# Kernel tuning notes

Measured on AMD Instinct MI355X. Metric: run time of the kernel, lower is better.

## Reference

```python
import jax, jax.numpy as jnp
import numpy as np
from jax import lax

L, B, T_IMG, T_TXT = 12, 2, 256, 64
E, H, G = 1024, 16, 2730
V = 16416  # image_vocab_count + 1
C = E // H
EPS = 1e-6  # flax LayerNorm default


def _ln(x, scale, bias):
    mu = jnp.mean(x, -1, keepdims=True)
    var = jnp.var(x, -1, keepdims=True)
    y = (x - mu) * lax.rsqrt(var + EPS)
    if scale is not None:
        y = y * scale
    if bias is not None:
        y = y + bias
    return y


def _attend(k, v, q, mask, o_w):
    # k,v: [B,K,H,C]  q: [B,Q,H,C]  mask: [B,K]
    bias = jnp.where(mask, 0.0, -jnp.inf)[:, None, None, :]
    w = jnp.einsum('bqhc,bkhc->bhqk', q, k) + bias
    w = jax.nn.softmax(w, axis=-1)
    out = jnp.einsum('bhqk,bkhc->bqhc', w, v)
    return out.reshape(out.shape[0], out.shape[1], E) @ o_w


def setup_inputs():
    key = jax.random.key(0)
    ks = jax.random.split(key, 16)
    s = 0.02
    n = lambda k, shape: jax.random.normal(k, shape, jnp.float32) * s
    return dict(
        encoder_state=n(ks[0], (B, T_TXT, E)),
        keys_state=jnp.zeros((L, B, T_IMG, H, C), jnp.float32),
        values_state=jnp.zeros((L, B, T_IMG, H, C), jnp.float32),
        attention_mask=jnp.ones((B, T_TXT), jnp.bool_),
        prev_token=5000,
        token_index=100,
        embed_tok=n(ks[1], (V, E)),
        embed_pos=n(ks[2], (T_IMG, E)),
        ln_emb_s=jnp.ones((E,), jnp.float32),
        ln_emb_b=jnp.zeros((E,), jnp.float32),
        final_ln_b=jnp.zeros((E,), jnp.float32),
        lm_head_w=n(ks[3], (E, V)),
        pre_sa_ln_b=jnp.zeros((L, E), jnp.float32),
        sa_q_w=n(ks[4], (L, E, E)), sa_k_w=n(ks[5], (L, E, E)),
        sa_v_w=n(ks[6], (L, E, E)), sa_o_w=n(ks[7], (L, E, E)),
        sa_ln_s=jnp.ones((L, E), jnp.float32), sa_ln_b=jnp.zeros((L, E), jnp.float32),
        pre_ca_ln_b=jnp.zeros((L, E), jnp.float32),
        ca_q_w=n(ks[8], (L, E, E)), ca_k_w=n(ks[9], (L, E, E)),
        ca_v_w=n(ks[10], (L, E, E)), ca_o_w=n(ks[11], (L, E, E)),
        ca_ln_s=jnp.ones((L, E), jnp.float32), ca_ln_b=jnp.zeros((L, E), jnp.float32),
        glu_ln0_b=jnp.zeros((L, E), jnp.float32),
        glu_fc0_w=n(ks[12], (L, E, G)), glu_fc1_w=n(ks[13], (L, E, G)),
        glu_ln1_b=jnp.zeros((L, G), jnp.float32),
        glu_fc2_w=n(ks[14], (L, G, E)),
    )


def _decode_step(encoder_state, keys_state, values_state, attention_mask,
                 prev_token, token_index, embed_tok, embed_pos,
                 ln_emb_s, ln_emb_b, final_ln_b, lm_head_w, layer_params):
    ones = jnp.ones((B, 1), jnp.int32)
    ds = embed_tok[prev_token * ones] + embed_pos[token_index * ones]  # [B,1,E]
    ds = _ln(ds, ln_emb_s, ln_emb_b)
    self_mask = jnp.broadcast_to(jnp.arange(T_IMG) < token_index + 1, (B, T_IMG))
    scale = C ** 0.5

    def step(ds, xs):
        ks_l, vs_l, p = xs  # per-layer KV cache [B,T_IMG,H,C] and params
        (pre_sa_b, qw, kw, vw, ow, sa_s, sa_b,
         pre_ca_b, cqw, ckw, cvw, cow, ca_s, ca_b,
         g0b, f0, f1, g1b, f2) = p
        # --- self attention with KV-cache append ---
        residual = ds
        x = _ln(ds, None, pre_sa_b)
        ks_l = lax.dynamic_update_slice(ks_l, (x @ kw).reshape(B, 1, H, C), (0, token_index, 0, 0))
        vs_l = lax.dynamic_update_slice(vs_l, (x @ vw).reshape(B, 1, H, C), (0, token_index, 0, 0))
        q = (x @ qw).reshape(B, 1, H, C) / scale
        x = _attend(ks_l, vs_l, q, self_mask, ow)
        ds = residual + _ln(x, sa_s, sa_b)
        # --- cross attention over encoder state ---
        residual = ds
        x = _ln(ds, None, pre_ca_b)
        ek = (encoder_state @ ckw).reshape(B, T_TXT, H, C)
        ev = (encoder_state @ cvw).reshape(B, T_TXT, H, C)
        q = (x @ cqw).reshape(B, 1, H, C) / scale
        x = _attend(ek, ev, q, attention_mask, cow)
        ds = residual + _ln(x, ca_s, ca_b)
        # --- GLU FFN ---
        residual = ds
        z = _ln(ds, None, g0b)
        w = jax.nn.gelu(z @ f0, approximate=False)
        z = _ln(w * (z @ f1), None, g1b)
        ds = residual + z @ f2
        return ds, (ks_l, vs_l)

    ds, (keys_state, values_state) = lax.scan(step, ds, (keys_state, values_state, layer_params))
    ds = _ln(ds, None, final_ln_b)
    logits = ds @ lm_head_w  # [B,1,V]
    return logits, keys_state, values_state


def reference(encoder_state, keys_state, values_state, attention_mask, prev_token,
              token_index, embed_tok, embed_pos, ln_emb_s, ln_emb_b, final_ln_b,
              lm_head_w, pre_sa_ln_b, sa_q_w, sa_k_w, sa_v_w, sa_o_w, sa_ln_s,
              sa_ln_b, pre_ca_ln_b, ca_q_w, ca_k_w, ca_v_w, ca_o_w, ca_ln_s,
              ca_ln_b, glu_ln0_b, glu_fc0_w, glu_fc1_w, glu_ln1_b, glu_fc2_w):
    layer_params = (pre_sa_ln_b, sa_q_w, sa_k_w, sa_v_w, sa_o_w, sa_ln_s, sa_ln_b,
                    pre_ca_ln_b, ca_q_w, ca_k_w, ca_v_w, ca_o_w, ca_ln_s, ca_ln_b,
                    glu_ln0_b, glu_fc0_w, glu_fc1_w, glu_ln1_b, glu_fc2_w)
    return _decode_step(encoder_state, keys_state, values_state, attention_mask,
                        prev_token, token_index, embed_tok, embed_pos,
                        ln_emb_s, ln_emb_b, final_ln_b, lm_head_w, layer_params)
```

## Files before the change

kernel.cpp:

```cpp
#include <hip/hip_runtime.h>
#include <math.h>

#define LAYERS 12
#define EE 1024
#define GG 2730
#define VV 16416
#define EPS 1e-6f

#define OFF_DS 0
#define NSLOT 37
#define OFF_ACC (OFF_DS + NSLOT*2048)
#define ACC_STRIDE 28672
#define AQ 0
#define AK 2048
#define AV 4096
#define AY 6144
#define ASC 10240
#define AY2 14336
#define AA 16384
#define AB2 21844
#define ACC_TOTAL (LAYERS*ACC_STRIDE)

#define KVL 524288
#define KVB 262144

struct MegaP {
  const float* enc; const float* keys_in; const float* values_in;
  const int* maski; const int* pt; const int* ti;
  const float* tok; const float* pos; const float* ln_s; const float* ln_b;
  const float* final_b; const float* lm_w;
  const float* pre_sa_b; const float* saq; const float* sak; const float* sav;
  const float* sao; const float* sas; const float* sab;
  const float* pre_ca_b; const float* caq; const float* ckw; const float* cvw;
  const float* cao; const float* cas; const float* cab;
  const float* g0b; const float* f0; const float* f1; const float* g1b; const float* f2;
  float* logits; float* keys_out; float* values_out; float* ws;
};

__device__ __forceinline__ void red4(float* sm, float& a, float& b, float& c, float& d){
  #pragma unroll
  for(int o=32;o;o>>=1){ a+=__shfl_down(a,o); b+=__shfl_down(b,o); c+=__shfl_down(c,o); d+=__shfl_down(d,o); }
  int w=threadIdx.x>>6, l=threadIdx.x&63;
  __syncthreads();
  if(l==0){ sm[w]=a; sm[4+w]=b; sm[8+w]=c; sm[12+w]=d; }
  __syncthreads();
  a=sm[0]+sm[1]+sm[2]+sm[3]; b=sm[4]+sm[5]+sm[6]+sm[7];
  c=sm[8]+sm[9]+sm[10]+sm[11]; d=sm[12]+sm[13]+sm[14]+sm[15];
}

__device__ __forceinline__ void ln_stats_g(const float* v, int K, float* sm,
    float& mu0, float& rs0, float& mu1, float& rs1){
  float s0=0,q0=0,s1=0,q1=0;
  for(int i=threadIdx.x;i<K;i+=256){ float a=v[i], b=v[K+i]; s0+=a;q0+=a*a;s1+=b;q1+=b*b; }
  red4(sm,s0,q0,s1,q1);
  mu0=s0/K; mu1=s1/K;
  rs0=rsqrtf(fmaxf(q0/K-mu0*mu0,0.f)+EPS);
  rs1=rsqrtf(fmaxf(q1/K-mu1*mu1,0.f)+EPS);
}

__device__ __forceinline__ void ln_stats_l(float (*Ds)[1024], float* sm,
    float& mu0, float& rs0, float& mu1, float& rs1){
  float s0=0,q0=0,s1=0,q1=0;
  for(int i=threadIdx.x;i<EE;i+=256){ float a=Ds[0][i], b=Ds[1][i]; s0+=a;q0+=a*a;s1+=b;q1+=b*b; }
  red4(sm,s0,q0,s1,q1);
  mu0=s0/EE; mu1=s1/EE;
  rs0=rsqrtf(fmaxf(q0/EE-mu0*mu0,0.f)+EPS);
  rs1=rsqrtf(fmaxf(q1/EE-mu1*mu1,0.f)+EPS);
}

__device__ __forceinline__ void build_ds3(const float* dsi, const float* accL,
    const float* sasl, const float* sabl, const float* casl, const float* cabl,
    float (*Ds)[1024], float* sm){
  float mu0,rs0,mu1,rs1;
  ln_stats_g(accL+AY, EE, sm, mu0,rs0,mu1,rs1);
  for(int i=threadIdx.x;i<EE;i+=256){ float sc=sasl[i], bi=sabl[i];
    Ds[0][i]=dsi[i]    + (accL[AY+i]-mu0)*rs0*sc + bi;
    Ds[1][i]=dsi[EE+i] + (accL[AY+EE+i]-mu1)*rs1*sc + bi; }
  ln_stats_g(accL+AY2, EE, sm, mu0,rs0,mu1,rs1);
  for(int i=threadIdx.x;i<EE;i+=256){ float sc=casl[i], bi=cabl[i];
    Ds[0][i] += (accL[AY2+i]-mu0)*rs0*sc + bi;
    Ds[1][i] += (accL[AY2+EE+i]-mu1)*rs1*sc + bi; }
}

__global__ __launch_bounds__(256)
void k_prelude(MegaP p){
  __shared__ float ev[EE];
  __shared__ float sm[16];
  const int t=threadIdx.x, b=blockIdx.x;
  if (b==0){
    int ptv = p.pt[0], tiv = p.ti[0];
    float s0=0,q0=0,d1=0,d2=0;
    for(int i=t;i<EE;i+=256){ float v=p.tok[(size_t)ptv*EE+i]+p.pos[(size_t)tiv*EE+i]; ev[i]=v; s0+=v; q0+=v*v; }
    red4(sm,s0,q0,d1,d2);
    float mu=s0/EE, rs=rsqrtf(fmaxf(q0/EE-mu*mu,0.f)+EPS);
    float* ds0 = p.ws + OFF_DS;
    __syncthreads();
    for(int i=t;i<EE;i+=256){ float y=(ev[i]-mu)*rs*p.ln_s[i]+p.ln_b[i]; ds0[i]=y; ds0[EE+i]=y; }
  } else {
    int idx = (b-1)*256 + t;
    for (int i=idx; i<2*VV; i+=9984) p.logits[i]=0.f;
    float* a0 = p.ws + OFF_ACC;
    for (int i=idx; i<ACC_STRIDE; i+=9984) a0[i]=0.f;
    float* d3 = p.ws + OFF_DS + 3*2048;
    for (int i=idx; i<2048; i+=9984) d3[i]=0.f;
  }
}

__global__ __launch_bounds__(256)
void k_qkv(MegaP p, int l){
  __shared__ float Xs[2][1024];
  __shared__ float sm[16];
  const int t=threadIdx.x, bx=blockIdx.x, by=blockIdx.y;
  if (bx >= 12){
    int cb = (bx-12)*64 + by;
    #pragma unroll
    for(int j=0;j<4;j++){
      int idx4 = cb*1024 + j*256 + t;
      int kv = idx4 >> 17;
      int r4 = idx4 & 131071;
      size_t off = (size_t)l*KVL + (size_t)r4*4;
      float4 v = *(const float4*)((kv? p.values_in : p.keys_in) + off);
      *(float4*)((kv? p.values_out : p.keys_out) + off) = v;
    }
    if (l < 11){
      int zi = cb*256 + t;
      float* an = p.ws + OFF_ACC + (size_t)(l+1)*ACC_STRIDE;
      if (zi < ACC_STRIDE) an[zi]=0.f;
      float* dn = p.ws + OFF_DS + (size_t)(3*l+6)*2048;
      if (zi < 2048) dn[zi]=0.f;
    }
    return;
  }
  const float* dsi = p.ws + OFF_DS + (size_t)(3*l)*2048;
  float* accL = p.ws + OFF_ACC + (size_t)l*ACC_STRIDE;
  const size_t lE2=(size_t)l*EE*EE, lE=(size_t)l*EE;
  int c = bx*256 + t;
  int sel = c>>10, cc = c&1023;
  const float* W = (sel==0? p.saq : sel==1? p.sak : p.sav) + lE2;
  float* O = accL + (sel==0? AQ : sel==1? AK : AV);
  int k0 = by*16;
  const float* wp = W + (size_t)k0*EE + cc;
  float wr[16];
  #pragma unroll
  for(int k=0;k<16;k++) wr[k] = wp[(size_t)k*EE];
  float mu0,rs0,mu1,rs1;
  ln_stats_g(dsi, EE, sm, mu0,rs0,mu1,rs1);
  for(int i=t;i<EE;i+=256){ float bi=p.pre_sa_b[lE+i];
    Xs[0][i]=(dsi[i]-mu0)*rs0+bi; Xs[1][i]=(dsi[EE+i]-mu1)*rs1+bi; }
  __syncthreads();
  float a0=0,a1=0;
  #pragma unroll
  for(int k=0;k<16;k++){ a0+=Xs[0][k0+k]*wr[k]; a1+=Xs[1][k0+k]*wr[k]; }
  atomicAdd(&O[cc],a0); atomicAdd(&O[EE+cc],a1);
}

__global__ __launch_bounds__(256)
void k_selfo(MegaP p, int l){
  __shared__ float Ds[2][1024];
  __shared__ float att[2][256];
  __shared__ float sm[16];
  const int t=threadIdx.x, bkid=blockIdx.x, tiv=p.ti[0];
  float* accL = p.ws + OFF_ACC + (size_t)l*ACC_STRIDE;
  const size_t lE2=(size_t)l*EE*EE;
  int cg=bkid&3, h=(bkid>>2)&15, sub=(bkid>>6)&3, hoff=h*64;
  if (t < 128){ int bb2=t>>6, c2=t&63; Ds[bb2][c2] = accL[AQ + bb2*EE + hoff + c2]*0.125f; }
  __syncthreads();
  for(int bb2=0;bb2<2;bb2++)
    for(int tt=t; tt<=tiv; tt+=256){
      const float* kr = (tt<tiv) ? (p.keys_in + (size_t)l*KVL + (size_t)bb2*KVB + (size_t)tt*EE + hoff)
                                 : (accL + AK + bb2*EE + hoff);
      float d=0;
      #pragma unroll
      for(int c2=0;c2<64;c2++) d += Ds[bb2][c2]*kr[c2];
      att[bb2][tt] = d;
    }
  __syncthreads();
  int wv=t>>6, l2=t&63;
  if (wv<2){
    float m=-3.4e38f;
    for(int tt=l2; tt<=tiv; tt+=64) m=fmaxf(m, att[wv][tt]);
    #pragma unroll
    for(int o=32;o;o>>=1) m=fmaxf(m,__shfl_xor(m,o));
    float s=0;
    for(int tt=l2; tt<=tiv; tt+=64){ float e=__expf(att[wv][tt]-m); att[wv][tt]=e; s+=e; }
    #pragma unroll
    for(int o=32;o;o>>=1) s+=__shfl_xor(s,o);
    if(l2==0) sm[8+wv]=1.f/s;
  }
  __syncthreads();
  {
    int bb2=t>>7, j=(t>>3)&15, part=t&7, colh=sub*16+j;
    float v=0;
    for(int tt=part; tt<=tiv; tt+=8){
      float vv = (tt<tiv)? p.values_in[(size_t)l*KVL + (size_t)bb2*KVB + (size_t)tt*EE + hoff + colh]
                         : accL[AV + bb2*EE + hoff + colh];
      v += att[bb2][tt]*vv;
    }
    v += __shfl_down(v,4,8); v += __shfl_down(v,2,8); v += __shfl_down(v,1,8);
    if(part==0) Ds[bb2][512+j] = v*sm[8+bb2];
  }
  __syncthreads();
  {
    int c = cg*256+t, kb = hoff + sub*16;
    const float* wp = p.sao + lE2 + (size_t)kb*EE + c;
    float a0=0,a1=0;
    #pragma unroll
    for(int j2=0;j2<16;j2++){ float w=wp[(size_t)j2*EE]; a0+=Ds[0][512+j2]*w; a1+=Ds[1][512+j2]*w; }
    atomicAdd(&accL[AY+c],a0); atomicAdd(&accL[AY+EE+c],a1);
  }
  if (cg==0 && sub==0){
    int bb2=t>>7, kv=(t>>6)&1, c2=t&63;
    float val = accL[(kv?AV:AK) + bb2*EE + hoff + c2];
    float* dst = (kv? p.values_out : p.keys_out)
               + (size_t)l*KVL + (size_t)bb2*KVB + (size_t)tiv*EE + hoff + c2;
    *dst = val;
  }
}

__global__ __launch_bounds__(256)
void k_qscore(MegaP p, int l){
  __shared__ float Xs[1024];
  __shared__ float P[16][64];
  __shared__ float qs[64];
  __shared__ float us[256];
  __shared__ float sm[16];
  const int t=threadIdx.x, bh=blockIdx.x, ec=blockIdx.y;
  const int b=bh>>4, h=bh&15, hoff=h*64;
  float* accL = p.ws + OFF_ACC + (size_t)l*ACC_STRIDE;
  const float* dsi = p.ws + OFF_DS + (size_t)(3*l)*2048;
  const size_t lE2=(size_t)l*EE*EE, lE=(size_t)l*EE;
  const int w=t>>6, ln=t&63;

  float s0=0,q0=0;
  for(int i=t;i<EE;i+=256){ float v=accL[AY+b*EE+i]; s0+=v; q0+=v*v; }
  #pragma unroll
  for(int o=32;o;o>>=1){ s0+=__shfl_down(s0,o); q0+=__shfl_down(q0,o); }
  if(ln==0){ sm[w]=s0; sm[4+w]=q0; }
  __syncthreads();
  float mu=(sm[0]+sm[1]+sm[2]+sm[3])/EE;
  float qq=(sm[4]+sm[5]+sm[6]+sm[7])/EE;
  float rs=rsqrtf(fmaxf(qq-mu*mu,0.f)+EPS);
  float s1=0,q1=0;
  for(int i=t;i<EE;i+=256){
    float d = dsi[b*EE+i] + (accL[AY+b*EE+i]-mu)*rs*p.sas[lE+i] + p.sab[lE+i];
    Xs[i]=d; s1+=d; q1+=d*d;
  }
  #pragma unroll
  for(int o=32;o;o>>=1){ s1+=__shfl_down(s1,o); q1+=__shfl_down(q1,o); }
  if(ln==0){ sm[8+w]=s1; sm[12+w]=q1; }
  __syncthreads();
  float mu2=(sm[8]+sm[9]+sm[10]+sm[11])/EE;
  float q2=(sm[12]+sm[13]+sm[14]+sm[15])/EE;
  float rs2=rsqrtf(fmaxf(q2-mu2*mu2,0.f)+EPS);
  for(int i=t;i<EE;i+=256) Xs[i] = (Xs[i]-mu2)*rs2 + p.pre_ca_b[lE+i];
  __syncthreads();

  {
    int c4=t&15, kr=t>>4;
    const float4* cq = (const float4*)(p.caq + lE2 + (size_t)kr*EE + hoff) + c4;
    float ax=0,ay=0,az=0,aw=0;
    #pragma unroll 8
    for(int i=0;i<64;i++){
      float4 wv = cq[(size_t)i*16*256];
      float x = Xs[kr+16*i];
      ax+=x*wv.x; ay+=x*wv.y; az+=x*wv.z; aw+=x*wv.w;
    }
    P[kr][c4*4+0]=ax; P[kr][c4*4+1]=ay; P[kr][c4*4+2]=az; P[kr][c4*4+3]=aw;
  }
  __syncthreads();
  if (t<64){
    float qv=0;
    #pragma unroll
    for(int kr=0;kr<16;kr++) qv += P[kr][t];
    qs[t] = qv*0.125f;
  }
  __syncthreads();

  {
    const float4* ckp = (const float4*)(p.ckw + lE2 + (size_t)(ec*256+t)*EE + hoff);
    float u=0;
    #pragma unroll
    for(int j=0;j<16;j++){
      float4 wv=ckp[j];
      u += wv.x*qs[4*j] + wv.y*qs[4*j+1] + wv.z*qs[4*j+2] + wv.w*qs[4*j+3];
    }
    us[t]=u;
  }
  __syncthreads();

  int t2=t&63, q4=t>>6;
  const float4* ep = (const float4*)(p.enc + (size_t)(b*64+t2)*EE + ec*256 + q4*64);
  float pa=0;
  #pragma unroll
  for(int j=0;j<16;j++){
    float4 e4=ep[j];
    pa += e4.x*us[q4*64+4*j] + e4.y*us[q4*64+4*j+1] + e4.z*us[q4*64+4*j+2] + e4.w*us[q4*64+4*j+3];
  }
  atomicAdd(&accL[ASC + (b*16+h)*64 + t2], pa);
}

__global__ __launch_bounds__(256)
void k_ovy2(MegaP p, int l){
  __shared__ float att[64];
  __shared__ float ctxp[2][128];
  __shared__ float ctxs[128];
  __shared__ float P[256];
  __shared__ float outh[64];
  const int t=threadIdx.x, bh=blockIdx.x, es=blockIdx.y;
  const int b=bh>>4, h=bh&15, hoff=h*64, e0=es*128;
  float* accL = p.ws + OFF_ACC + (size_t)l*ACC_STRIDE;
  const size_t lE2=(size_t)l*EE*EE;
  const int c=t&63, part=t>>6;
  const float* vp = p.cvw + lE2 + (size_t)(e0+part*32)*EE + hoff + c;
  float wr[32];
  #pragma unroll
  for(int j=0;j<32;j++) wr[j] = vp[(size_t)j*EE];
  if (t<64){
    float sc = accL[ASC + (b*16+h)*64 + t];
    int mi=b*64+t;
    bool valid = (p.maski[mi]!=0) || (((const unsigned char*)p.maski)[mi]!=0);
    sc = valid? sc : -3.4e38f;
    float m=sc;
    #pragma unroll
    for(int o=32;o;o>>=1) m=fmaxf(m,__shfl_xor(m,o));
    float e_ = valid? __expf(sc-m) : 0.f;
    float s=e_;
    #pragma unroll
    for(int o=32;o;o>>=1) s+=__shfl_xor(s,o);
    att[t]=e_/s;
  }
  __syncthreads();
  {
    int e2=t>>1, half=t&1;
    const float* ep = p.enc + (size_t)(b*64+half*32)*EE + e0+e2;
    float ca=0;
    #pragma unroll 8
    for(int tt=0;tt<32;tt++) ca += att[half*32+tt]*ep[(size_t)tt*EE];
    ctxp[half][e2]=ca;
  }
  __syncthreads();
  if (t<128) ctxs[t] = ctxp[0][t]+ctxp[1][t];
  __syncthreads();
  {
    float po=0;
    #pragma unroll
    for(int j=0;j<32;j++) po += ctxs[part*32+j]*wr[j];
    P[t]=po;
  }
  __syncthreads();
  if (t<64) outh[t] = P[t]+P[64+t]+P[128+t]+P[192+t];
  __syncthreads();
  {
    const float* cop = p.cao + lE2 + (size_t)hoff*EE;
    for(int n=t;n<EE;n+=256){
      float y=0;
      #pragma unroll 8
      for(int c2=0;c2<64;c2++) y += outh[c2]*cop[(size_t)c2*EE + n];
      atomicAdd(&accL[AY2 + b*EE + n], y);
    }
  }
}

__global__ __launch_bounds__(256)
void k_glu01(MegaP p, int l){
  __shared__ float Xs[2][1024];
  __shared__ float Ds[2][1024];
  __shared__ float sm[16];
  const int t=threadIdx.x;
  const float* dsi = p.ws + OFF_DS + (size_t)(3*l)*2048;
  float* accL = p.ws + OFF_ACC + (size_t)l*ACC_STRIDE;
  const size_t lEG=(size_t)l*EE*GG, lE=(size_t)l*EE;
  int c2 = blockIdx.x*256 + t;
  int k0 = blockIdx.y*16;
  int sel=0, col=0;
  const float* W = nullptr;
  float2 wr[16];
  if (c2 < 2730){
    sel = (c2>=1365); int cc2 = sel? c2-1365 : c2; col = cc2*2;
    W = (sel? p.f1 : p.f0) + lEG;
    const float2* wp = (const float2*)(W + (size_t)k0*GG + col);
    #pragma unroll
    for(int k=0;k<16;k++) wr[k] = wp[(size_t)k*1365];
  }
  build_ds3(dsi, accL, p.sas+lE, p.sab+lE, p.cas+lE, p.cab+lE, Ds, sm);
  float mu0,rs0,mu1,rs1;
  ln_stats_l(Ds, sm, mu0,rs0,mu1,rs1);
  for(int i=t;i<EE;i+=256){ float bi=p.g0b[lE+i];
    Xs[0][i]=(Ds[0][i]-mu0)*rs0+bi; Xs[1][i]=(Ds[1][i]-mu1)*rs1+bi; }
  __syncthreads();
  if (c2 < 2730){
    float* O = accL + (sel? AB2 : AA);
    float a0=0,a1=0,b0=0,b1=0;
    #pragma unroll
    for(int k=0;k<16;k++){
      float x0=Xs[0][k0+k], x1=Xs[1][k0+k];
      a0+=x0*wr[k].x; a1+=x0*wr[k].y; b0+=x1*wr[k].x; b1+=x1*wr[k].y;
    }
    atomicAdd(&O[col+0],a0); atomicAdd(&O[col+1],a1);
    atomicAdd(&O[GG+col+0],b0); atomicAdd(&O[GG+col+1],b1);
  }
}

__global__ __launch_bounds__(256)
void k_glu2(MegaP p, int l){
  __shared__ float Xs[2][2736];
  __shared__ float Ds[2][1024];
  __shared__ float sm[16];
  const int t=threadIdx.x;
  const float* dsi = p.ws + OFF_DS + (size_t)(3*l)*2048;
  float* ds4 = p.ws + OFF_DS + (size_t)(3*l+3)*2048;
  float* accL = p.ws + OFF_ACC + (size_t)l*ACC_STRIDE;
  const size_t lGE=(size_t)l*GG*EE, lE=(size_t)l*EE, lG=(size_t)l*GG;
  const int ks = blockIdx.y;
  int c = blockIdx.x*256 + t;
  int k0 = ks*32, k1 = k0+32; if (k1>GG) k1=GG;
  const float* wp = p.f2 + lGE + (size_t)k0*EE + c;
  float wr[32];
  #pragma unroll
  for(int k=0;k<32;k++) wr[k] = (k0+k<GG) ? wp[(size_t)k*EE] : 0.f;
  if (ks==0) build_ds3(dsi, accL, p.sas+lE, p.sab+lE, p.cas+lE, p.cab+lE, Ds, sm);
  float s0=0,q0=0,s1=0,q1=0;
  for(int i=t;i<GG;i+=256){
    float a0v=accL[AA+i], a1v=accL[AA+GG+i];
    float b0v=accL[AB2+i], b1v=accL[AB2+GG+i];
    float g0v=0.5f*a0v*(1.f+erff(a0v*0.70710678118654752f));
    float g1v=0.5f*a1v*(1.f+erff(a1v*0.70710678118654752f));
    float t0=g0v*b0v, t1=g1v*b1v;
    Xs[0][i]=t0; Xs[1][i]=t1;
    s0+=t0;q0+=t0*t0;s1+=t1;q1+=t1*t1;
  }
  red4(sm,s0,q0,s1,q1);
  float mu0=s0/GG, mu1=s1/GG;
  float rs0=rsqrtf(fmaxf(q0/GG-mu0*mu0,0.f)+EPS), rs1=rsqrtf(fmaxf(q1/GG-mu1*mu1,0.f)+EPS);
  for(int i=t;i<GG;i+=256){ float bi=p.g1b[lG+i];
    Xs[0][i]=(Xs[0][i]-mu0)*rs0+bi; Xs[1][i]=(Xs[1][i]-mu1)*rs1+bi; }
  __syncthreads();
  float a0=0,b0=0;
  if (ks==0){ a0=Ds[0][c]; b0=Ds[1][c]; }
  #pragma unroll
  for(int k=0;k<32;k++){
    if (k0+k<GG){ a0+=Xs[0][k0+k]*wr[k]; b0+=Xs[1][k0+k]*wr[k]; }
  }
  atomicAdd(&ds4[c],a0); atomicAdd(&ds4[EE+c],b0);
}

__global__ __launch_bounds__(256)
void k_lm(MegaP p){
  __shared__ float Xs[2][1024];
  __shared__ float sm[16];
  const int t=threadIdx.x;
  const float* dsf = p.ws + OFF_DS + (size_t)36*2048;
  float mu0,rs0,mu1,rs1;
  ln_stats_g(dsf, EE, sm, mu0,rs0,mu1,rs1);
  for(int i=t;i<EE;i+=256){ float bi=p.final_b[i];
    Xs[0][i]=(dsf[i]-mu0)*rs0+bi; Xs[1][i]=(dsf[EE+i]-mu1)*rs1+bi; }
  __syncthreads();
  int c4 = blockIdx.x*256 + t;
  if (c4 < 4104){
    int col = c4*4;
    int k0 = blockIdx.y*32;
    const float4* wp = (const float4*)(p.lm_w + (size_t)k0*VV + col);
    float a0=0,a1=0,a2=0,a3=0,b0=0,b1=0,b2=0,b3=0;
    #pragma unroll 8
    for(int k=0;k<32;k++){
      float4 w=*wp; wp+=4104;
      float x0=Xs[0][k0+k], x1=Xs[1][k0+k];
      a0+=x0*w.x; a1+=x0*w.y; a2+=x0*w.z; a3+=x0*w.w;
      b0+=x1*w.x; b1+=x1*w.y; b2+=x1*w.z; b3+=x1*w.w;
    }
    atomicAdd(&p.logits[col+0],a0); atomicAdd(&p.logits[col+1],a1);
    atomicAdd(&p.logits[col+2],a2); atomicAdd(&p.logits[col+3],a3);
    atomicAdd(&p.logits[VV+col+0],b0); atomicAdd(&p.logits[VV+col+1],b1);
    atomicAdd(&p.logits[VV+col+2],b2); atomicAdd(&p.logits[VV+col+3],b3);
  }
}

extern "C" void kernel_launch(void* const* d_in, const int* in_sizes, int n_in,
                              void* d_out, int out_size, void* d_ws, size_t ws_size,
                              hipStream_t stream){
  (void)in_sizes; (void)n_in; (void)out_size; (void)ws_size;
  float* out = (float*)d_out;
  float* ws = (float*)d_ws;

  MegaP P;
  P.enc        = (const float*)d_in[0];
  P.keys_in    = (const float*)d_in[1];
  P.values_in  = (const float*)d_in[2];
  P.maski      = (const int*)d_in[3];
  P.pt         = (const int*)d_in[4];
  P.ti         = (const int*)d_in[5];
  P.tok        = (const float*)d_in[6];
  P.pos        = (const float*)d_in[7];
  P.ln_s       = (const float*)d_in[8];
  P.ln_b       = (const float*)d_in[9];
  P.final_b    = (const float*)d_in[10];
  P.lm_w       = (const float*)d_in[11];
  P.pre_sa_b   = (const float*)d_in[12];
  P.saq        = (const float*)d_in[13];
  P.sak        = (const float*)d_in[14];
  P.sav        = (const float*)d_in[15];
  P.sao        = (const float*)d_in[16];
  P.sas        = (const float*)d_in[17];
  P.sab        = (const float*)d_in[18];
  P.pre_ca_b   = (const float*)d_in[19];
  P.caq        = (const float*)d_in[20];
  P.ckw        = (const float*)d_in[21];
  P.cvw        = (const float*)d_in[22];
  P.cao        = (const float*)d_in[23];
  P.cas        = (const float*)d_in[24];
  P.cab        = (const float*)d_in[25];
  P.g0b        = (const float*)d_in[26];
  P.f0         = (const float*)d_in[27];
  P.f1         = (const float*)d_in[28];
  P.g1b        = (const float*)d_in[29];
  P.f2         = (const float*)d_in[30];
  P.logits     = out;
  P.keys_out   = out + (size_t)2*VV;
  P.values_out = P.keys_out + (size_t)LAYERS*KVL;
  P.ws         = ws;

  k_prelude<<<40,256,0,stream>>>(P);
  for (int l=0;l<LAYERS;l++){
    k_qkv   <<<dim3(16,64),256,0,stream>>>(P,l);
    k_selfo <<<256,        256,0,stream>>>(P,l);
    k_qscore<<<dim3(32,4), 256,0,stream>>>(P,l);
    k_ovy2  <<<dim3(32,8), 256,0,stream>>>(P,l);
    k_glu01 <<<dim3(11,64),256,0,stream>>>(P,l);
    k_glu2  <<<dim3(4,86), 256,0,stream>>>(P,l);
  }
  k_lm<<<dim3(17,32),256,0,stream>>>(P);
}
```

Baseline: 1.237 ms.

## Precompute cross-attention encoder K/V projections and overlap them with GLU kernels

Cross-attention keys and values (encoder_state times the K/V weights) are now computed explicitly as small 128x1024 GEMMs stored in workspace. Layer 0 is computed in the prelude, and each later layer's are computed by extra blocks appended to the previous layer's GLU kernels. The query-score and output kernels merge into one k_cross2 kernel that reads the precomputed K/V. This removes the reassociated per-head weight-times-query products and one launch per layer. In exchange it adds extra tiled GEMM work and about 12MB of workspace traffic, and the naive 32x32 shared-memory tiles may be slow.

After: 3.185 ms. 2.57x slower.

```diff
diff --git a/kernel.cpp b/kernel.cpp
--- a/kernel.cpp
+++ b/kernel.cpp
@@ -7,7 +7,9 @@
 #define VV 16416
 #define EPS 1e-6f
 
-#define OFF_DS 0
+#define OFF_EK 0
+#define OFF_EV 1572864
+#define OFF_DS 3145728
 #define NSLOT 37
 #define OFF_ACC (OFF_DS + NSLOT*2048)
 #define ACC_STRIDE 28672
@@ -15,7 +17,6 @@
 #define AK 2048
 #define AV 4096
 #define AY 6144
-#define ASC 10240
 #define AY2 14336
 #define AA 16384
 #define AB2 21844
@@ -82,10 +83,36 @@
     Ds[1][i] += (accL[AY2+EE+i]-mu1)*rs1*sc + bi; }
 }
 
+__device__ __forceinline__ void ekev_tile(const MegaP& p, int ll, int proj, int rt, int ct,
+                                          float (*As)[33], float (*Bs)[33]){
+  const int t=threadIdx.x;
+  const float* W = (proj? p.cvw : p.ckw) + (size_t)ll*EE*EE;
+  float* out = p.ws + (proj? OFF_EV : OFF_EK) + (size_t)ll*128*EE;
+  const int r0 = rt*32, c0 = ct*32;
+  const int r = t>>3, c8 = t&7;
+  float acc0=0,acc1=0,acc2=0,acc3=0;
+  for (int k0=0;k0<EE;k0+=32){
+    for (int i=t;i<1024;i+=256){ int rr=i>>5, k=i&31; As[rr][k] = p.enc[(size_t)(r0+rr)*EE + k0+k]; }
+    for (int i=t;i<1024;i+=256){ int k=i>>5, c=i&31; Bs[k][c] = W[(size_t)(k0+k)*EE + c0+c]; }
+    __syncthreads();
+    #pragma unroll 8
+    for (int k=0;k<32;k++){
+      float a = As[r][k];
+      acc0+=a*Bs[k][c8*4+0]; acc1+=a*Bs[k][c8*4+1];
+      acc2+=a*Bs[k][c8*4+2]; acc3+=a*Bs[k][c8*4+3];
+    }
+    __syncthreads();
+  }
+  float* op = out + (size_t)(r0+r)*EE + c0 + c8*4;
+  op[0]=acc0; op[1]=acc1; op[2]=acc2; op[3]=acc3;
+}
+
 __global__ __launch_bounds__(256)
 void k_prelude(MegaP p){
   __shared__ float ev[EE];
   __shared__ float sm[16];
+  __shared__ float As[32][33];
+  __shared__ float Bs[32][33];
   const int t=threadIdx.x, b=blockIdx.x;
   if (b==0){
     int ptv = p.pt[0], tiv = p.ti[0];
@@ -96,13 +123,17 @@
     float* ds0 = p.ws + OFF_DS;
     __syncthreads();
     for(int i=t;i<EE;i+=256){ float y=(ev[i]-mu)*rs*p.ln_s[i]+p.ln_b[i]; ds0[i]=y; ds0[EE+i]=y; }
-  } else {
+  } else if (b < 40){
     int idx = (b-1)*256 + t;
     for (int i=idx; i<2*VV; i+=9984) p.logits[i]=0.f;
     float* a0 = p.ws + OFF_ACC;
     for (int i=idx; i<ACC_STRIDE; i+=9984) a0[i]=0.f;
     float* d3 = p.ws + OFF_DS + 3*2048;
     for (int i=idx; i<2048; i+=9984) d3[i]=0.f;
+  } else {
+    int id = b-40;
+    int proj = id>>7, tid = id&127;
+    ekev_tile(p, 0, proj, tid>>5, tid&31, As, Bs);
   }
 }
 
@@ -218,13 +249,15 @@
 }
 
 __global__ __launch_bounds__(256)
-void k_qscore(MegaP p, int l){
+void k_cross2(MegaP p, int l){
   __shared__ float Xs[1024];
-  __shared__ float P[16][64];
+  __shared__ float Pq[1024];
+  __shared__ float P2[256];
   __shared__ float qs[64];
-  __shared__ float us[256];
-  __shared__ float sm[16];
-  const int t=threadIdx.x, bh=blockIdx.x, ec=blockIdx.y;
+  __shared__ float att[64];
+  __shared__ float outh[64];
+  __shared__ float sm[16];
+  const int t=threadIdx.x, bh=blockIdx.x, half=blockIdx.y;
   const int b=bh>>4, h=bh&15, hoff=h*64;
   float* accL = p.ws + OFF_ACC + (size_t)l*ACC_STRIDE;
   const float* dsi = p.ws + OFF_DS + (size_t)(3*l)*2048;
@@ -265,94 +298,63 @@
       float x = Xs[kr+16*i];
       ax+=x*wv.x; ay+=x*wv.y; az+=x*wv.z; aw+=x*wv.w;
     }
-    P[kr][c4*4+0]=ax; P[kr][c4*4+1]=ay; P[kr][c4*4+2]=az; P[kr][c4*4+3]=aw;
+    Pq[kr*64+c4*4+0]=ax; Pq[kr*64+c4*4+1]=ay; Pq[kr*64+c4*4+2]=az; Pq[kr*64+c4*4+3]=aw;
   }
   __syncthreads();
   if (t<64){
     float qv=0;
     #pragma unroll
-    for(int kr=0;kr<16;kr++) qv += P[kr][t];
+    for(int kr=0;kr<16;kr++) qv += Pq[kr*64+t];
     qs[t] = qv*0.125f;
   }
   __syncthreads();
 
   {
-    const float4* ckp = (const float4*)(p.ckw + lE2 + (size_t)(ec*256+t)*EE + hoff);
-    float u=0;
-    #pragma unroll
-    for(int j=0;j<16;j++){
-      float4 wv=ckp[j];
-      u += wv.x*qs[4*j] + wv.y*qs[4*j+1] + wv.z*qs[4*j+2] + wv.w*qs[4*j+3];
-    }
-    us[t]=u;
-  }
-  __syncthreads();
-
-  int t2=t&63, q4=t>>6;
-  const float4* ep = (const float4*)(p.enc + (size_t)(b*64+t2)*EE + ec*256 + q4*64);
-  float pa=0;
-  #pragma unroll
-  for(int j=0;j<16;j++){
-    float4 e4=ep[j];
-    pa += e4.x*us[q4*64+4*j] + e4.y*us[q4*64+4*j+1] + e4.z*us[q4*64+4*j+2] + e4.w*us[q4*64+4*j+3];
-  }
-  atomicAdd(&accL[ASC + (b*16+h)*64 + t2], pa);
-}
-
-__global__ __launch_bounds__(256)
-void k_ovy2(MegaP p, int l){
-  __shared__ float att[64];
-  __shared__ float ctxp[2][128];
-  __shared__ float ctxs[128];
-  __shared__ float P[256];
-  __shared__ float outh[64];
-  const int t=threadIdx.x, bh=blockIdx.x, es=blockIdx.y;
-  const int b=bh>>4, h=bh&15, hoff=h*64, e0=es*128;
-  float* accL = p.ws + OFF_ACC + (size_t)l*ACC_STRIDE;
-  const size_t lE2=(size_t)l*EE*EE;
-  const int c=t&63, part=t>>6;
-  const float* vp = p.cvw + lE2 + (size_t)(e0+part*32)*EE + hoff + c;
-  float wr[32];
-  #pragma unroll
-  for(int j=0;j<32;j++) wr[j] = vp[(size_t)j*EE];
+    int tt=t&63, q4=t>>6;
+    const float4* ekp = (const float4*)(p.ws + OFF_EK
+        + ((size_t)l*128 + b*64 + tt)*EE + hoff + q4*16);
+    float pa=0;
+    #pragma unroll
+    for(int j=0;j<4;j++){
+      float4 e4=ekp[j];
+      pa += e4.x*qs[q4*16+4*j] + e4.y*qs[q4*16+4*j+1]
+          + e4.z*qs[q4*16+4*j+2] + e4.w*qs[q4*16+4*j+3];
+    }
+    P2[t]=pa;
+  }
+  __syncthreads();
   if (t<64){
-    float sc = accL[ASC + (b*16+h)*64 + t];
+    float sc = P2[t]+P2[64+t]+P2[128+t]+P2[192+t];
     int mi=b*64+t;
     bool valid = (p.maski[mi]!=0) || (((const unsigned char*)p.maski)[mi]!=0);
     sc = valid? sc : -3.4e38f;
     float m=sc;
     #pragma unroll
     for(int o=32;o;o>>=1) m=fmaxf(m,__shfl_xor(m,o));
-    float e_ = valid? __expf(sc-m) : 0.f;
+    float e_=valid? __expf(sc-m):0.f;
     float s=e_;
     #pragma unroll
     for(int o=32;o;o>>=1) s+=__shfl_xor(s,o);
     att[t]=e_/s;
   }
   __syncthreads();
+
   {
-    int e2=t>>1, half=t&1;
-    const float* ep = p.enc + (size_t)(b*64+half*32)*EE + e0+e2;
-    float ca=0;
-    #pragma unroll 8
-    for(int tt=0;tt<32;tt++) ca += att[half*32+tt]*ep[(size_t)tt*EE];
-    ctxp[half][e2]=ca;
-  }
-  __syncthreads();
-  if (t<128) ctxs[t] = ctxp[0][t]+ctxp[1][t];
-  __syncthreads();
+    int c=t&63, part=t>>6;
+    const float* evp = p.ws + OFF_EV + ((size_t)l*128 + b*64 + part*16)*EE + hoff + c;
+    float po=0;
+    #pragma unroll
+    for(int j=0;j<16;j++) po += att[part*16+j]*evp[(size_t)j*EE];
+    P2[t]=po;
+  }
+  __syncthreads();
+  if (t<64) outh[t] = P2[t]+P2[64+t]+P2[128+t]+P2[192+t];
+  __syncthreads();
+
   {
-    float po=0;
-    #pragma unroll
-    for(int j=0;j<32;j++) po += ctxs[part*32+j]*wr[j];
-    P[t]=po;
-  }
-  __syncthreads();
-  if (t<64) outh[t] = P[t]+P[64+t]+P[128+t]+P[192+t];
-  __syncthreads();
-  {
+    int n0 = half*512;
     const float* cop = p.cao + lE2 + (size_t)hoff*EE;
-    for(int n=t;n<EE;n+=256){
+    for(int n=n0+t; n<n0+512; n+=256){
       float y=0;
       #pragma unroll 8
       for(int c2=0;c2<64;c2++) y += outh[c2]*cop[(size_t)c2*EE + n];
@@ -366,12 +368,21 @@
   __shared__ float Xs[2][1024];
   __shared__ float Ds[2][1024];
   __shared__ float sm[16];
-  const int t=threadIdx.x;
+  __shared__ float As[32][33];
+  __shared__ float Bs[32][33];
+  const int t=threadIdx.x, bk=blockIdx.x;
+  if (bk >= 704){
+    if (l < 11){
+      int id = bk-704;
+      ekev_tile(p, l+1, 0, id>>5, id&31, As, Bs);
+    }
+    return;
+  }
   const float* dsi = p.ws + OFF_DS + (size_t)(3*l)*2048;
   float* accL = p.ws + OFF_ACC + (size_t)l*ACC_STRIDE;
   const size_t lEG=(size_t)l*EE*GG, lE=(size_t)l*EE;
-  int c2 = blockIdx.x*256 + t;
-  int k0 = blockIdx.y*16;
+  int c2 = (bk%11)*256 + t;
+  int k0 = (bk/11)*16;
   int sel=0, col=0;
   const float* W = nullptr;
   float2 wr[16];
@@ -406,14 +417,23 @@
   __shared__ float Xs[2][2736];
   __shared__ float Ds[2][1024];
   __shared__ float sm[16];
-  const int t=threadIdx.x;
+  __shared__ float As[32][33];
+  __shared__ float Bs[32][33];
+  const int t=threadIdx.x, bk=blockIdx.x;
+  if (bk >= 344){
+    if (l < 11){
+      int id = bk-344;
+      ekev_tile(p, l+1, 1, id>>5, id&31, As, Bs);
+    }
+    return;
+  }
   const float* dsi = p.ws + OFF_DS + (size_t)(3*l)*2048;
   float* ds4 = p.ws + OFF_DS + (size_t)(3*l+3)*2048;
   float* accL = p.ws + OFF_ACC + (size_t)l*ACC_STRIDE;
   const size_t lGE=(size_t)l*GG*EE, lE=(size_t)l*EE, lG=(size_t)l*GG;
-  const int ks = blockIdx.y;
-  int c = blockIdx.x*256 + t;
-  int k0 = ks*32, k1 = k0+32; if (k1>GG) k1=GG;
+  const int ks = bk>>2;
+  int c = (bk&3)*256 + t;
+  int k0 = ks*32;
   const float* wp = p.f2 + lGE + (size_t)k0*EE + c;
   float wr[32];
   #pragma unroll
@@ -519,14 +539,13 @@
   P.values_out = P.keys_out + (size_t)LAYERS*KVL;
   P.ws         = ws;
 
-  k_prelude<<<40,256,0,stream>>>(P);
+  k_prelude<<<296,256,0,stream>>>(P);
   for (int l=0;l<LAYERS;l++){
     k_qkv   <<<dim3(16,64),256,0,stream>>>(P,l);
     k_selfo <<<256,        256,0,stream>>>(P,l);
-    k_qscore<<<dim3(32,4), 256,0,stream>>>(P,l);
-    k_ovy2  <<<dim3(32,8), 256,0,stream>>>(P,l);
-    k_glu01 <<<dim3(11,64),256,0,stream>>>(P,l);
-    k_glu2  <<<dim3(4,86), 256,0,stream>>>(P,l);
+    k_cross2<<<dim3(32,2), 256,0,stream>>>(P,l);
+    k_glu01 <<<832,        256,0,stream>>>(P,l);
+    k_glu2  <<<472,        256,0,stream>>>(P,l);
   }
   k_lm<<<dim3(17,32),256,0,stream>>>(P);
 }
```
